# Kernel optimization log

Measured on AMD Instinct MI355X. Metric: run time of the kernel, lower is better.

The kernel has to match this reference:

```python
import jax, jax.numpy as jnp
import numpy as np

B, S, D, H, MLP = 2, 2048, 1024, 16, 4096
DH = D // H
EPS_LN = 1e-6
KERNEL_EPS = 1e-3  # fast_attention generalized kernel_epsilon


def layer_norm(x, scale, bias):
    m = jnp.mean(x, axis=-1, keepdims=True)
    v = jnp.mean(jnp.square(x - m), axis=-1, keepdims=True)
    return (x - m) * jax.lax.rsqrt(v + EPS_LN) * scale + bias


def performer_causal_attention(q, k, v):
    """FAVOR+ generalized attention (deterministic relu features), causal.

    q,k,v: [B,S,H,DH]. phi(x) = relu(x) + eps. Linear-time via prefix sums:
      out_i = phi(q_i) . cumsum_j<=i phi(k_j) v_j^T / (phi(q_i) . cumsum phi(k_j))
    """
    phi_q = jax.nn.relu(q) + KERNEL_EPS          # [B,S,H,M]
    phi_k = jax.nn.relu(k) + KERNEL_EPS          # [B,S,H,M]
    kv = jnp.cumsum(jnp.einsum('bshm,bshd->bshmd', phi_k, v), axis=1)  # [B,S,H,M,DH]
    num = jnp.einsum('bshm,bshmd->bshd', phi_q, kv)
    den = jnp.einsum('bshm,bshm->bsh', phi_q, jnp.cumsum(phi_k, axis=1))
    return num / den[..., None]


def setup_inputs() -> dict:
    key = jax.random.key(0)
    ks = jax.random.split(key, 7)
    def w(k, shape, scale):
        return jax.random.normal(k, shape, jnp.float32) * scale
    s_in = 1.0 / np.sqrt(D)
    return {
        'inputs': jax.random.normal(ks[0], (B, S, D), jnp.float32),
        'ln1_scale': jnp.ones((D,), jnp.float32),
        'ln1_bias': jnp.zeros((D,), jnp.float32),
        'wq': w(ks[1], (D, H, DH), s_in),
        'wk': w(ks[2], (D, H, DH), s_in),
        'wv': w(ks[3], (D, H, DH), s_in),
        'wo': w(ks[4], (H, DH, D), s_in),
        'ln2_scale': jnp.ones((D,), jnp.float32),
        'ln2_bias': jnp.zeros((D,), jnp.float32),
        'w1': w(ks[5], (D, MLP), s_in),
        'b1': jnp.zeros((MLP,), jnp.float32),
        'w2': w(ks[6], (MLP, D), 1.0 / np.sqrt(MLP)),
        'b2': jnp.zeros((D,), jnp.float32),
    }


def reference(inputs, ln1_scale, ln1_bias, wq, wk, wv, wo,
              ln2_scale, ln2_bias, w1, b1, w2, b2):
    # pre-LN self-attention (Performer FAVOR+ generalized, causal)
    x = layer_norm(inputs, ln1_scale, ln1_bias)
    q = jnp.einsum('bsd,dhm->bshm', x, wq)
    k = jnp.einsum('bsd,dhm->bshm', x, wk)
    v = jnp.einsum('bsd,dhm->bshm', x, wv)
    attn = performer_causal_attention(q, k, v)          # [B,S,H,DH]
    attn_out = jnp.einsum('bshm,hmd->bsd', attn, wo)    # output projection
    x = attn_out + inputs                               # residual
    # pre-LN MLP block
    y = layer_norm(x, ln2_scale, ln2_bias)
    y = jax.nn.gelu(y @ w1 + b1) @ w2 + b2
    return x + y
```

## Files before the change

### kernel.cpp

```cpp
#include <hip/hip_runtime.h>
#include <math.h>
#include <stdint.h>

typedef __bf16 bf16;
typedef bf16  bf16x8 __attribute__((ext_vector_type(8)));
typedef float f32x4  __attribute__((ext_vector_type(4)));

constexpr int Bb  = 2;
constexpr int Ss  = 2048;
constexpr int Dd  = 1024;
constexpr int Hh  = 16;
constexpr int DHh = 64;
constexpr int MLPd = 4096;
constexpr int ROWS = Bb * Ss;
constexpr int NC  = Ss / 64;
constexpr int BH  = Bb * Hh;
constexpr float EPS_LN = 1e-6f;
constexpr float KEPS   = 1e-3f;

__device__ __forceinline__ void async_copy16(const bf16* g, bf16* l) {
    __builtin_amdgcn_global_load_lds(
        (__attribute__((address_space(1))) void*)g,
        (__attribute__((address_space(3))) void*)l,
        16, 0, 0);
}

__device__ __forceinline__ int swz64(int row, int col) {
    return row * 64 + (((col >> 3) ^ row) & 7) * 8 + (col & 7);
}

__global__ __launch_bounds__(256) void preproc_kernel(
    const float* __restrict__ inputs,
    const float* __restrict__ ln1_scale, const float* __restrict__ ln1_bias,
    bf16* __restrict__ xln, bf16* __restrict__ inp_bf,
    const float* __restrict__ wq, const float* __restrict__ wk,
    const float* __restrict__ wv, const float* __restrict__ wo,
    bf16* __restrict__ wqT, bf16* __restrict__ wkT,
    bf16* __restrict__ wvT, bf16* __restrict__ woT,
    const float* __restrict__ w1, bf16* __restrict__ w1T,
    const float* __restrict__ w2, bf16* __restrict__ w2T)
{
    __shared__ float tile[32][33];
    __shared__ float ssum[4], ssq[4];
    const int blk = blockIdx.x;
    const int sector = blk >> 12;

    if (sector == 0) {
        const int row = blk;
        const float* xr = inputs + (size_t)row * Dd;
        const int c0 = threadIdx.x * 4;
        float vals[4];
        float sum = 0.f, sumsq = 0.f;
#pragma unroll
        for (int i = 0; i < 4; i++) {
            float v = xr[c0 + i];
            vals[i] = v;
            sum += v;
            sumsq += v * v;
        }
#pragma unroll
        for (int off = 32; off > 0; off >>= 1) {
            sum   += __shfl_down(sum, off);
            sumsq += __shfl_down(sumsq, off);
        }
        const int wave = threadIdx.x >> 6;
        if ((threadIdx.x & 63) == 0) { ssum[wave] = sum; ssq[wave] = sumsq; }
        __syncthreads();
        const float tot   = ssum[0] + ssum[1] + ssum[2] + ssum[3];
        const float totsq = ssq[0] + ssq[1] + ssq[2] + ssq[3];
        const float mean = tot * (1.f / Dd);
        const float var  = totsq * (1.f / Dd) - mean * mean;
        const float r = rsqrtf(var + EPS_LN);
        bf16* orow = xln + (size_t)row * Dd;
        bf16* irow = inp_bf + (size_t)row * Dd;
#pragma unroll
        for (int i = 0; i < 4; i++) {
            irow[c0 + i] = (bf16)vals[i];
            orow[c0 + i] = (bf16)((vals[i] - mean) * r * ln1_scale[c0 + i] + ln1_bias[c0 + i]);
        }
    } else {
        const float* in; bf16* out; int K, N, bx, by;
        if (sector == 1) {
            const int local = blk - 4096;
            const int z = local >> 10;
            in  = (z == 0) ? wq : (z == 1) ? wk : (z == 2) ? wv : wo;
            out = (z == 0) ? wqT : (z == 1) ? wkT : (z == 2) ? wvT : woT;
            K = 1024; N = 1024;
            bx = local & 31; by = (local >> 5) & 31;
        } else if (sector == 2) {
            const int local = blk - 8192;
            in = w1; out = w1T; K = 1024; N = 4096;
            bx = local & 127; by = local >> 7;
        } else {
            const int local = blk - 12288;
            in = w2; out = w2T; K = 4096; N = 1024;
            bx = local & 31; by = local >> 5;
        }
        const int k0 = by * 32, n0 = bx * 32;
        const int tx = threadIdx.x & 31, ty = threadIdx.x >> 5;
#pragma unroll
        for (int i = 0; i < 32; i += 8)
            tile[ty + i][tx] = in[(size_t)(k0 + ty + i) * N + n0 + tx];
        __syncthreads();
#pragma unroll
        for (int i = 0; i < 32; i += 8)
            out[(size_t)(n0 + ty + i) * K + k0 + tx] = (bf16)tile[tx][ty + i];
    }
}

__global__ __launch_bounds__(256) void ln_kernel(const bf16* __restrict__ x,
                                                 const float* __restrict__ scale,
                                                 const float* __restrict__ bias,
                                                 bf16* __restrict__ out)
{
    const int row = blockIdx.x;
    const bf16* xr = x + (size_t)row * Dd;
    const int c0 = threadIdx.x * 4;
    float vals[4];
    float sum = 0.f, sumsq = 0.f;
#pragma unroll
    for (int i = 0; i < 4; i++) {
        float v = (float)xr[c0 + i];
        vals[i] = v;
        sum += v;
        sumsq += v * v;
    }
#pragma unroll
    for (int off = 32; off > 0; off >>= 1) {
        sum   += __shfl_down(sum, off);
        sumsq += __shfl_down(sumsq, off);
    }
    __shared__ float ssum[4], ssq[4];
    const int wave = threadIdx.x >> 6;
    if ((threadIdx.x & 63) == 0) { ssum[wave] = sum; ssq[wave] = sumsq; }
    __syncthreads();
    const float tot   = ssum[0] + ssum[1] + ssum[2] + ssum[3];
    const float totsq = ssq[0] + ssq[1] + ssq[2] + ssq[3];
    const float mean = tot * (1.f / Dd);
    const float var  = totsq * (1.f / Dd) - mean * mean;
    const float r = rsqrtf(var + EPS_LN);
    bf16* orow = out + (size_t)row * Dd;
#pragma unroll
    for (int i = 0; i < 4; i++)
        orow[c0 + i] = (bf16)((vals[i] - mean) * r * scale[c0 + i] + bias[c0 + i]);
}

enum { EP_QKV = 0, EP_NONE = 1, EP_RES = 2, EP_GELU = 3, EP_BIAS_RES = 4 };

template <int TN, int BK, int NDIM, int KDIM, int MODE>
__global__ __launch_bounds__(256, 2) void mfma_gemm(const bf16* __restrict__ A,
                                                    const bf16* __restrict__ BT,
                                                    void* __restrict__ Cout,
                                                    const float* __restrict__ bias,
                                                    const void* __restrict__ res,
                                                    bf16* __restrict__ out2,
                                                    bf16* __restrict__ out3)
{
    constexpr int WCT = TN / 2;
    constexpr int NJ  = TN / 32;
    constexpr int NS  = BK / 32;
    constexpr int CPR = BK / 8;
    constexpr int RPI = 2048 / BK;
    constexpr int GRIDY = 32;
    constexpr int RPX = GRIDY / 8;
    __shared__ bf16 As[128 * BK];
    __shared__ bf16 Bs[TN * BK];
    const int t = threadIdx.x;
    const int wave = t >> 6, lane = t & 63;

    const int bid = blockIdx.x;
    const int xcd = bid & 7, idx = bid >> 3;
    const int row0 = (xcd * RPX + (idx & (RPX - 1))) * 128;
    const int col0 = (idx / RPX) * TN;

    const int wr = wave >> 1, wc = wave & 1;

    const int srow = t / CPR;
    const int gch  = (t % CPR) ^ (srow & 7);
    const int sdst = t * 8;

    const bf16* gA = A  + (size_t)(row0 + srow) * KDIM + gch * 8;
    const bf16* gB = BT + (size_t)(col0 + srow) * KDIM + gch * 8;

    const int m = lane & 15, quad = lane >> 4;
    const int mx7 = m & 7;

    f32x4 acc[4][NJ] = {};

    for (int k0 = 0; k0 < KDIM; k0 += BK) {
        __syncthreads();
#pragma unroll
        for (int i = 0; i < 128 / RPI; i++)
            async_copy16(gA + (size_t)i * RPI * KDIM, &As[i * 2048 + sdst]);
#pragma unroll
        for (int i = 0; i < TN / RPI; i++)
            async_copy16(gB + (size_t)i * RPI * KDIM, &Bs[i * 2048 + sdst]);
        __syncthreads();

#pragma unroll
        for (int s = 0; s < NS; s++) {
            const int pco = ((s * 4 + quad) ^ mx7) * 8;
            bf16x8 aF[4], bF[NJ];
#pragma unroll
            for (int i = 0; i < 4; i++)
                aF[i] = *(const bf16x8*)&As[(wr * 64 + i * 16 + m) * BK + pco];
#pragma unroll
            for (int j = 0; j < NJ; j++)
                bF[j] = *(const bf16x8*)&Bs[(wc * WCT + j * 16 + m) * BK + pco];
#pragma unroll
            for (int i = 0; i < 4; i++)
#pragma unroll
                for (int j = 0; j < NJ; j++)
                    acc[i][j] = __builtin_amdgcn_mfma_f32_16x16x32_bf16(
                        aF[i], bF[j], acc[i][j], 0, 0, 0);
        }
        gA += BK;
        gB += BK;
    }

    bf16* qkv_dst = nullptr;
    int col_base = col0;
    bool do_phi = false;
    if constexpr (MODE == EP_QKV) {
        const int third = col0 >> 10;
        qkv_dst = (third == 0) ? (bf16*)Cout : (third == 1) ? out2 : out3;
        col_base = col0 & 1023;
        do_phi = (third < 2);
    }

#pragma unroll
    for (int i = 0; i < 4; i++) {
#pragma unroll
        for (int j = 0; j < NJ; j++) {
#pragma unroll
            for (int r = 0; r < 4; r++) {
                const int row = row0 + wr * 64 + i * 16 + quad * 4 + r;
                const int col = col0 + wc * WCT + j * 16 + m;
                float val = acc[i][j][r];
                if constexpr (MODE == EP_QKV) {
                    const int lc = col_base + wc * WCT + j * 16 + m;
                    if (do_phi) val = fmaxf(val, 0.f) + KEPS;
                    qkv_dst[(size_t)row * 1024 + lc] = (bf16)val;
                } else if constexpr (MODE == EP_NONE) {
                    ((bf16*)Cout)[(size_t)row * NDIM + col] = (bf16)val;
                } else if constexpr (MODE == EP_RES) {
                    val += (float)((const bf16*)res)[(size_t)row * NDIM + col];
                    ((bf16*)Cout)[(size_t)row * NDIM + col] = (bf16)val;
                } else if constexpr (MODE == EP_GELU) {
                    val += bias[col];
                    const float u = 0.7978845608028654f * (val + 0.044715f * val * val * val);
                    const float e = __expf(2.f * u);
                    val = val * (1.f - 1.f / (e + 1.f));
                    ((bf16*)Cout)[(size_t)row * NDIM + col] = (bf16)val;
                } else {
                    val += bias[col] + (float)((const bf16*)res)[(size_t)row * NDIM + col];
                    ((float*)Cout)[(size_t)row * NDIM + col] = val;
                }
            }
        }
    }
}

__global__ __launch_bounds__(256) void chunk_kv_kernel(const bf16* __restrict__ phik,
                                                       const bf16* __restrict__ v,
                                                       bf16* __restrict__ kvs,
                                                       float* __restrict__ ksums)
{
    const int c = blockIdx.x, bh = blockIdx.y;
    const int b = bh >> 4, h = bh & 15;
    __shared__ bf16 Kt[64 * 64];
    __shared__ bf16 Vt[64 * 64];
    const int t = threadIdx.x;
    const int wave = t >> 6, lane = t & 63;
    const int m16 = lane & 15, quad = lane >> 4;
    const int wr = wave >> 1, wc = wave & 1;
    const int f = t & 63, s4 = t >> 6;

#pragma unroll
    for (int i = 0; i < 16; i++) {
        const int s = s4 + 4 * i;
        const size_t g = ((size_t)((b * Ss + c * 64 + s) * Hh + h)) * DHh + f;
        Kt[swz64(f, s)] = phik[g];
        Vt[swz64(f, s)] = v[g];
    }
    __syncthreads();

    f32x4 acc[2][2] = {};
#pragma unroll
    for (int ks = 0; ks < 2; ks++) {
        bf16x8 aF[2], bF[2];
#pragma unroll
        for (int i = 0; i < 2; i++)
            aF[i] = *(const bf16x8*)&Kt[swz64(wr * 32 + i * 16 + m16, ks * 32 + quad * 8)];
#pragma unroll
        for (int j = 0; j < 2; j++)
            bF[j] = *(const bf16x8*)&Vt[swz64(wc * 32 + j * 16 + m16, ks * 32 + quad * 8)];
#pragma unroll
        for (int i = 0; i < 2; i++)
#pragma unroll
            for (int j = 0; j < 2; j++)
                acc[i][j] = __builtin_amdgcn_mfma_f32_16x16x32_bf16(
                    aF[i], bF[j], acc[i][j], 0, 0, 0);
    }

    const size_t base = ((size_t)bh * NC + c) * 4096;
#pragma unroll
    for (int i = 0; i < 2; i++)
#pragma unroll
        for (int j = 0; j < 2; j++)
#pragma unroll
            for (int r = 0; r < 4; r++) {
                const int mrow = wr * 32 + i * 16 + quad * 4 + r;
                const int dcol = wc * 32 + j * 16 + m16;
                kvs[base + mrow * 64 + dcol] = (bf16)acc[i][j][r];
            }

    if (t < 64) {
        float s_ = 0.f;
#pragma unroll
        for (int p = 0; p < 8; p++) {
            bf16x8 k8 = *(const bf16x8*)&Kt[t * 64 + p * 8];
#pragma unroll
            for (int e = 0; e < 8; e++) s_ += (float)k8[e];
        }
        ksums[((size_t)bh * NC + c) * 64 + t] = s_;
    }
}

__global__ __launch_bounds__(256) void scan_kernel(bf16* __restrict__ kvs,
                                                   float* __restrict__ ksums)
{
    const int e  = blockIdx.x * 256 + threadIdx.x;
    const int bh = blockIdx.y;
    float run = 0.f;
#pragma unroll 4
    for (int c = 0; c < NC; c++) {
        const size_t idx = ((size_t)bh * NC + c) * 4096 + e;
        const float val = (float)kvs[idx];
        kvs[idx] = (bf16)run;
        run += val;
    }
    if (blockIdx.x == 0 && threadIdx.x < 64) {
        float r = 0.f;
        for (int c = 0; c < NC; c++) {
            const size_t idx = ((size_t)bh * NC + c) * 64 + threadIdx.x;
            const float val = ksums[idx];
            ksums[idx] = r;
            r += val;
        }
    }
}

__global__ __launch_bounds__(256) void attn_out_kernel(const bf16* __restrict__ phiq,
                                                       const bf16* __restrict__ phik,
                                                       const bf16* __restrict__ v,
                                                       const bf16* __restrict__ kvs,
                                                       const float* __restrict__ ksums,
                                                       bf16* __restrict__ attn)
{
    const int c = blockIdx.x, bh = blockIdx.y;
    const int b = bh >> 4, h = bh & 15;
    __shared__ bf16 Qs [64 * 64];
    __shared__ bf16 KVb[64 * 64];
    __shared__ bf16 Sm [64 * 64];
    __shared__ bf16 KVt[64 * 64];
    __shared__ float ksm[64], den[64];
    const int t = threadIdx.x;
    const int wave = t >> 6, lane = t & 63;
    const int m16 = lane & 15, quad = lane >> 4;
    const int wr = wave >> 1, wc = wave & 1;
    const int f = t & 63, s4 = t >> 6;

#pragma unroll
    for (int i = 0; i < 16; i++) {
        const int s = s4 + 4 * i;
        const size_t g = ((size_t)((b * Ss + c * 64 + s) * Hh + h)) * DHh + f;
        Qs [swz64(s, f)] = phiq[g];
        KVb[swz64(s, f)] = phik[g];
    }
    if (t < 64) ksm[t] = ksums[((size_t)bh * NC + c) * 64 + t];
    __syncthreads();

    f32x4 sacc[2][2] = {};
#pragma unroll
    for (int ks = 0; ks < 2; ks++) {
        bf16x8 aF[2], bF[2];
#pragma unroll
        for (int i = 0; i < 2; i++)
            aF[i] = *(const bf16x8*)&Qs [swz64(wr * 32 + i * 16 + m16, ks * 32 + quad * 8)];
#pragma unroll
        for (int j = 0; j < 2; j++)
            bF[j] = *(const bf16x8*)&KVb[swz64(wc * 32 + j * 16 + m16, ks * 32 + quad * 8)];
#pragma unroll
        for (int i = 0; i < 2; i++)
#pragma unroll
            for (int j = 0; j < 2; j++)
                sacc[i][j] = __builtin_amdgcn_mfma_f32_16x16x32_bf16(
                    aF[i], bF[j], sacc[i][j], 0, 0, 0);
    }
#pragma unroll
    for (int i = 0; i < 2; i++)
#pragma unroll
        for (int j = 0; j < 2; j++)
#pragma unroll
            for (int r = 0; r < 4; r++) {
                const int row = wr * 32 + i * 16 + quad * 4 + r;
                const int col = wc * 32 + j * 16 + m16;
                Sm[swz64(row, col)] = (bf16)((col <= row) ? sacc[i][j][r] : 0.f);
            }
    __syncthreads();

#pragma unroll
    for (int i = 0; i < 16; i++) {
        const int s = s4 + 4 * i;
        const size_t g = ((size_t)((b * Ss + c * 64 + s) * Hh + h)) * DHh + f;
        KVb[swz64(f, s)] = v[g];
    }
    {
        const size_t base = ((size_t)bh * NC + c) * 4096;
#pragma unroll
        for (int i = 0; i < 16; i++) {
            const int e = t + 256 * i;
            KVt[swz64(e & 63, e >> 6)] = kvs[base + e];
        }
    }
    __syncthreads();

    if (t < 64) {
        float d_ = 0.f;
#pragma unroll
        for (int p = 0; p < 8; p++) {
            const int gc = (p ^ (t & 7)) * 8;
            bf16x8 q8 = *(const bf16x8*)&Qs[t * 64 + p * 8];
            bf16x8 s8 = *(const bf16x8*)&Sm[t * 64 + p * 8];
#pragma unroll
            for (int e = 0; e < 8; e++)
                d_ += (float)q8[e] * ksm[gc + e] + (float)s8[e];
        }
        den[t] = d_;
    }

    f32x4 oacc[2][2] = {};
#pragma unroll
    for (int ks = 0; ks < 2; ks++) {
        bf16x8 aF[2], bF[2];
#pragma unroll
        for (int i = 0; i < 2; i++)
            aF[i] = *(const bf16x8*)&Sm [swz64(wr * 32 + i * 16 + m16, ks * 32 + quad * 8)];
#pragma unroll
        for (int j = 0; j < 2; j++)
            bF[j] = *(const bf16x8*)&KVb[swz64(wc * 32 + j * 16 + m16, ks * 32 + quad * 8)];
#pragma unroll
        for (int i = 0; i < 2; i++)
#pragma unroll
            for (int j = 0; j < 2; j++)
                oacc[i][j] = __builtin_amdgcn_mfma_f32_16x16x32_bf16(
                    aF[i], bF[j], oacc[i][j], 0, 0, 0);
    }
#pragma unroll
    for (int ks = 0; ks < 2; ks++) {
        bf16x8 aF[2], bF[2];
#pragma unroll
        for (int i = 0; i < 2; i++)
            aF[i] = *(const bf16x8*)&Qs [swz64(wr * 32 + i * 16 + m16, ks * 32 + quad * 8)];
#pragma unroll
        for (int j = 0; j < 2; j++)
            bF[j] = *(const bf16x8*)&KVt[swz64(wc * 32 + j * 16 + m16, ks * 32 + quad * 8)];
#pragma unroll
        for (int i = 0; i < 2; i++)
#pragma unroll
            for (int j = 0; j < 2; j++)
                oacc[i][j] = __builtin_amdgcn_mfma_f32_16x16x32_bf16(
                    aF[i], bF[j], oacc[i][j], 0, 0, 0);
    }
    __syncthreads();

#pragma unroll
    for (int i = 0; i < 2; i++) {
#pragma unroll
        for (int r = 0; r < 4; r++) {
            const int row = wr * 32 + i * 16 + quad * 4 + r;
            const float dinv = 1.f / den[row];
#pragma unroll
            for (int j = 0; j < 2; j++) {
                const int col = wc * 32 + j * 16 + m16;
                attn[((size_t)((b * Ss + c * 64 + row) * Hh + h)) * DHh + col] =
                    (bf16)(oacc[i][j][r] * dinv);
            }
        }
    }
}

extern "C" void kernel_launch(void* const* d_in, const int* in_sizes, int n_in,
                              void* d_out, int out_size, void* d_ws, size_t ws_size,
                              hipStream_t stream)
{
    const float* inputs    = (const float*)d_in[0];
    const float* ln1_scale = (const float*)d_in[1];
    const float* ln1_bias  = (const float*)d_in[2];
    const float* wq        = (const float*)d_in[3];
    const float* wk        = (const float*)d_in[4];
    const float* wv        = (const float*)d_in[5];
    const float* wo        = (const float*)d_in[6];
    const float* ln2_scale = (const float*)d_in[7];
    const float* ln2_bias  = (const float*)d_in[8];
    const float* w1        = (const float*)d_in[9];
    const float* b1        = (const float*)d_in[10];
    const float* w2        = (const float*)d_in[11];
    const float* b2        = (const float*)d_in[12];
    float* out = (float*)d_out;

    char* ws = (char*)d_ws;
    bf16*  xln   = (bf16*)ws;
    bf16*  q     = (bf16*)(ws + (8ull  << 20));
    bf16*  k     = (bf16*)(ws + (16ull << 20));
    bf16*  v     = (bf16*)(ws + (24ull << 20));
    bf16*  kvs   = (bf16*)(ws + (32ull << 20));
    bf16*  x2    = (bf16*)(ws + (48ull << 20));
    bf16*  inp_bf= (bf16*)(ws + (56ull << 20));
    float* ksums = (float*)(ws + (64ull << 20));
    bf16*  wqT   = (bf16*)(ws + (64ull << 20) + (1ull << 18));
    bf16*  wkT   = wqT + 1024 * 1024;
    bf16*  wvT   = wkT + 1024 * 1024;
    bf16*  woT   = wvT + 1024 * 1024;
    bf16*  w1T   = woT + 1024 * 1024;
    bf16*  w2T   = w1T + 4096 * 1024;
    bf16*  attn  = xln;
    bf16*  yln   = q;
    bf16*  hbuf  = k;

    preproc_kernel<<<16384, 256, 0, stream>>>(
        inputs, ln1_scale, ln1_bias, xln, inp_bf,
        wq, wk, wv, wo, wqT, wkT, wvT, woT, w1, w1T, w2, w2T);

    mfma_gemm<256, 64, 3072, 1024, EP_QKV><<<dim3(12 * 32), 256, 0, stream>>>(
        xln, wqT, q, nullptr, nullptr, k, v);

    {
        dim3 gridA(NC, BH);
        chunk_kv_kernel<<<gridA, 256, 0, stream>>>(k, v, kvs, ksums);
        scan_kernel<<<dim3(4096 / 256, BH), 256, 0, stream>>>(kvs, ksums);
        attn_out_kernel<<<gridA, 256, 0, stream>>>(q, k, v, kvs, ksums, attn);
    }

    mfma_gemm<128, 64, 1024, 1024, EP_RES><<<dim3(8 * 32), 256, 0, stream>>>(
        attn, woT, x2, nullptr, inp_bf, nullptr, nullptr);

    ln_kernel<<<ROWS, 256, 0, stream>>>(x2, ln2_scale, ln2_bias, yln);

    mfma_gemm<256, 64, 4096, 1024, EP_GELU><<<dim3(16 * 32), 256, 0, stream>>>(
        yln, w1T, hbuf, b1, nullptr, nullptr, nullptr);
    mfma_gemm<128, 64, 1024, 4096, EP_BIAS_RES><<<dim3(8 * 32), 256, 0, stream>>>(
        hbuf, w2T, out, b2, x2, nullptr, nullptr);
}
```

Baseline: 309.3 us.

## Split-K the Wo and MLP2 GEMMs and fuse reductions into LN/epilogue

The Wo projection and second MLP GEMM, which had only 256 tiles, now use a two-way split-K so 512 blocks fill the GPU. Each half writes fp32 partials. The Wo partials are summed with the residual inside a fused reduce plus LayerNorm kernel that emits both x2 and the normalized input. The MLP2 partials are summed by a small reduce kernel that adds bias and residual. The QKV GEMM tile width also changes from 256 to 192 to give 512 blocks. This adds fp32 partial traffic and an extra launch in exchange for better occupancy.

Result: faster. 288.0 us (-6.9%).

```diff
diff --git a/kernel.cpp b/kernel.cpp
--- a/kernel.cpp
+++ b/kernel.cpp
@@ -108,19 +108,21 @@
     }
 }
 
-__global__ __launch_bounds__(256) void ln_kernel(const bf16* __restrict__ x,
-                                                 const float* __restrict__ scale,
-                                                 const float* __restrict__ bias,
-                                                 bf16* __restrict__ out)
+__global__ __launch_bounds__(256) void wo_reduce_ln(
+    const float* __restrict__ psA, const float* __restrict__ psB,
+    const bf16* __restrict__ inp,
+    const float* __restrict__ scale, const float* __restrict__ bias,
+    bf16* __restrict__ x2, bf16* __restrict__ yln)
 {
     const int row = blockIdx.x;
-    const bf16* xr = x + (size_t)row * Dd;
     const int c0 = threadIdx.x * 4;
+    const size_t base = (size_t)row * Dd + c0;
     float vals[4];
     float sum = 0.f, sumsq = 0.f;
 #pragma unroll
     for (int i = 0; i < 4; i++) {
-        float v = (float)xr[c0 + i];
+        float v = psA[base + i] + psB[base + i] + (float)inp[base + i];
+        v = (float)(bf16)v;
         vals[i] = v;
         sum += v;
         sumsq += v * v;
@@ -139,15 +141,31 @@
     const float mean = tot * (1.f / Dd);
     const float var  = totsq * (1.f / Dd) - mean * mean;
     const float r = rsqrtf(var + EPS_LN);
-    bf16* orow = out + (size_t)row * Dd;
-#pragma unroll
-    for (int i = 0; i < 4; i++)
-        orow[c0 + i] = (bf16)((vals[i] - mean) * r * scale[c0 + i] + bias[c0 + i]);
-}
-
-enum { EP_QKV = 0, EP_NONE = 1, EP_RES = 2, EP_GELU = 3, EP_BIAS_RES = 4 };
-
-template <int TN, int BK, int NDIM, int KDIM, int MODE>
+#pragma unroll
+    for (int i = 0; i < 4; i++) {
+        x2[base + i]  = (bf16)vals[i];
+        yln[base + i] = (bf16)((vals[i] - mean) * r * scale[c0 + i] + bias[c0 + i]);
+    }
+}
+
+__global__ __launch_bounds__(256) void mlp2_reduce(
+    float* __restrict__ outp, const float* __restrict__ psB,
+    const float* __restrict__ b2, const bf16* __restrict__ x2)
+{
+    const size_t i4 = ((size_t)blockIdx.x * 256 + threadIdx.x) * 4;
+    const int col = (int)(i4 & 1023);
+    f32x4 a = *(const f32x4*)&outp[i4];
+    f32x4 b = *(const f32x4*)&psB[i4];
+    f32x4 o;
+#pragma unroll
+    for (int j = 0; j < 4; j++)
+        o[j] = a[j] + b[j] + b2[col + j] + (float)x2[i4 + j];
+    *(f32x4*)&outp[i4] = o;
+}
+
+enum { EP_QKV = 0, EP_NONE = 1, EP_RES = 2, EP_GELU = 3, EP_BIAS_RES = 4, EP_PARTIAL = 5 };
+
+template <int TN, int BK, int NDIM, int KDIM, int MODE, int KSPLIT>
 __global__ __launch_bounds__(256, 2) void mfma_gemm(const bf16* __restrict__ A,
                                                     const bf16* __restrict__ BT,
                                                     void* __restrict__ Cout,
@@ -163,12 +181,16 @@
     constexpr int RPI = 2048 / BK;
     constexpr int GRIDY = 32;
     constexpr int RPX = GRIDY / 8;
+    constexpr int TILES = GRIDY * (NDIM / TN);
+    constexpr int KLEN  = KDIM / KSPLIT;
     __shared__ bf16 As[128 * BK];
     __shared__ bf16 Bs[TN * BK];
     const int t = threadIdx.x;
     const int wave = t >> 6, lane = t & 63;
 
-    const int bid = blockIdx.x;
+    const int bid0 = blockIdx.x;
+    const int ks  = (KSPLIT > 1) ? (bid0 / TILES) : 0;
+    const int bid = (KSPLIT > 1) ? (bid0 % TILES) : bid0;
     const int xcd = bid & 7, idx = bid >> 3;
     const int row0 = (xcd * RPX + (idx & (RPX - 1))) * 128;
     const int col0 = (idx / RPX) * TN;
@@ -179,15 +201,15 @@
     const int gch  = (t % CPR) ^ (srow & 7);
     const int sdst = t * 8;
 
-    const bf16* gA = A  + (size_t)(row0 + srow) * KDIM + gch * 8;
-    const bf16* gB = BT + (size_t)(col0 + srow) * KDIM + gch * 8;
+    const bf16* gA = A  + (size_t)(row0 + srow) * KDIM + ks * KLEN + gch * 8;
+    const bf16* gB = BT + (size_t)(col0 + srow) * KDIM + ks * KLEN + gch * 8;
 
     const int m = lane & 15, quad = lane >> 4;
     const int mx7 = m & 7;
 
     f32x4 acc[4][NJ] = {};
 
-    for (int k0 = 0; k0 < KDIM; k0 += BK) {
+    for (int k0 = 0; k0 < KLEN; k0 += BK) {
         __syncthreads();
 #pragma unroll
         for (int i = 0; i < 128 / RPI; i++)
@@ -216,16 +238,6 @@
         }
         gA += BK;
         gB += BK;
-    }
-
-    bf16* qkv_dst = nullptr;
-    int col_base = col0;
-    bool do_phi = false;
-    if constexpr (MODE == EP_QKV) {
-        const int third = col0 >> 10;
-        qkv_dst = (third == 0) ? (bf16*)Cout : (third == 1) ? out2 : out3;
-        col_base = col0 & 1023;
-        do_phi = (third < 2);
     }
 
 #pragma unroll
@@ -238,9 +250,10 @@
                 const int col = col0 + wc * WCT + j * 16 + m;
                 float val = acc[i][j][r];
                 if constexpr (MODE == EP_QKV) {
-                    const int lc = col_base + wc * WCT + j * 16 + m;
-                    if (do_phi) val = fmaxf(val, 0.f) + KEPS;
-                    qkv_dst[(size_t)row * 1024 + lc] = (bf16)val;
+                    const int third = col >> 10;
+                    bf16* dst = (third == 0) ? (bf16*)Cout : (third == 1) ? out2 : out3;
+                    if (third < 2) val = fmaxf(val, 0.f) + KEPS;
+                    dst[(size_t)row * 1024 + (col & 1023)] = (bf16)val;
                 } else if constexpr (MODE == EP_NONE) {
                     ((bf16*)Cout)[(size_t)row * NDIM + col] = (bf16)val;
                 } else if constexpr (MODE == EP_RES) {
@@ -252,9 +265,12 @@
                     const float e = __expf(2.f * u);
                     val = val * (1.f - 1.f / (e + 1.f));
                     ((bf16*)Cout)[(size_t)row * NDIM + col] = (bf16)val;
-                } else {
+                } else if constexpr (MODE == EP_BIAS_RES) {
                     val += bias[col] + (float)((const bf16*)res)[(size_t)row * NDIM + col];
                     ((float*)Cout)[(size_t)row * NDIM + col] = val;
+                } else {
+                    float* dst = (ks == 0) ? (float*)Cout : (float*)out2;
+                    dst[(size_t)row * NDIM + col] = val;
                 }
             }
         }
@@ -511,29 +527,32 @@
     float* out = (float*)d_out;
 
     char* ws = (char*)d_ws;
-    bf16*  xln   = (bf16*)ws;
-    bf16*  q     = (bf16*)(ws + (8ull  << 20));
-    bf16*  k     = (bf16*)(ws + (16ull << 20));
-    bf16*  v     = (bf16*)(ws + (24ull << 20));
-    bf16*  kvs   = (bf16*)(ws + (32ull << 20));
-    bf16*  x2    = (bf16*)(ws + (48ull << 20));
-    bf16*  inp_bf= (bf16*)(ws + (56ull << 20));
-    float* ksums = (float*)(ws + (64ull << 20));
-    bf16*  wqT   = (bf16*)(ws + (64ull << 20) + (1ull << 18));
-    bf16*  wkT   = wqT + 1024 * 1024;
-    bf16*  wvT   = wkT + 1024 * 1024;
-    bf16*  woT   = wvT + 1024 * 1024;
-    bf16*  w1T   = woT + 1024 * 1024;
-    bf16*  w2T   = w1T + 4096 * 1024;
-    bf16*  attn  = xln;
-    bf16*  yln   = q;
-    bf16*  hbuf  = k;
+    bf16*  xln    = (bf16*)ws;
+    bf16*  q      = (bf16*)(ws + (8ull  << 20));
+    bf16*  k      = (bf16*)(ws + (16ull << 20));
+    bf16*  v      = (bf16*)(ws + (24ull << 20));
+    bf16*  kvs    = (bf16*)(ws + (32ull << 20));
+    bf16*  x2     = (bf16*)(ws + (48ull << 20));
+    bf16*  inp_bf = (bf16*)(ws + (56ull << 20));
+    float* ksums  = (float*)(ws + (64ull << 20));
+    bf16*  wqT    = (bf16*)(ws + (64ull << 20) + (1ull << 18));
+    bf16*  wkT    = wqT + 1024 * 1024;
+    bf16*  wvT    = wkT + 1024 * 1024;
+    bf16*  woT    = wvT + 1024 * 1024;
+    bf16*  w1T    = woT + 1024 * 1024;
+    bf16*  w2T    = w1T + 4096 * 1024;
+    bf16*  attn   = xln;
+    bf16*  yln    = q;
+    bf16*  hbuf   = k;
+    float* psWo0  = (float*)(ws + (16ull << 20));
+    float* psWo1  = (float*)(ws + (32ull << 20));
+    float* psM2   = (float*)ws;
 
     preproc_kernel<<<16384, 256, 0, stream>>>(
         inputs, ln1_scale, ln1_bias, xln, inp_bf,
         wq, wk, wv, wo, wqT, wkT, wvT, woT, w1, w1T, w2, w2T);
 
-    mfma_gemm<256, 64, 3072, 1024, EP_QKV><<<dim3(12 * 32), 256, 0, stream>>>(
+    mfma_gemm<192, 64, 3072, 1024, EP_QKV, 1><<<dim3(512), 256, 0, stream>>>(
         xln, wqT, q, nullptr, nullptr, k, v);
 
     {
@@ -543,13 +562,17 @@
         attn_out_kernel<<<gridA, 256, 0, stream>>>(q, k, v, kvs, ksums, attn);
     }
 
-    mfma_gemm<128, 64, 1024, 1024, EP_RES><<<dim3(8 * 32), 256, 0, stream>>>(
-        attn, woT, x2, nullptr, inp_bf, nullptr, nullptr);
-
-    ln_kernel<<<ROWS, 256, 0, stream>>>(x2, ln2_scale, ln2_bias, yln);
-
-    mfma_gemm<256, 64, 4096, 1024, EP_GELU><<<dim3(16 * 32), 256, 0, stream>>>(
+    mfma_gemm<128, 64, 1024, 1024, EP_PARTIAL, 2><<<dim3(512), 256, 0, stream>>>(
+        attn, woT, psWo0, nullptr, nullptr, (bf16*)psWo1, nullptr);
+
+    wo_reduce_ln<<<ROWS, 256, 0, stream>>>(psWo0, psWo1, inp_bf,
+                                           ln2_scale, ln2_bias, x2, yln);
+
+    mfma_gemm<256, 64, 4096, 1024, EP_GELU, 1><<<dim3(512), 256, 0, stream>>>(
         yln, w1T, hbuf, b1, nullptr, nullptr, nullptr);
-    mfma_gemm<128, 64, 1024, 4096, EP_BIAS_RES><<<dim3(8 * 32), 256, 0, stream>>>(
-        hbuf, w2T, out, b2, x2, nullptr, nullptr);
-}
+
+    mfma_gemm<128, 64, 1024, 4096, EP_PARTIAL, 2><<<dim3(512), 256, 0, stream>>>(
+        hbuf, w2T, out, nullptr, nullptr, (bf16*)psM2, nullptr);
+
+    mlp2_reduce<<<4096, 256, 0, stream>>>(out, psM2, b2, x2);
+}
```
